# Performance work log

Measured on AMD Instinct MI355X. Metric: run time of the kernel, lower is better.

The kernel has to match this reference:

```python
import jax, jax.numpy as jnp
import numpy as np

B, L, D_MODEL = 2, 4096, 256
EXPAND = 2
D_INNER = EXPAND * D_MODEL
D_STATE = 16
D_CONV = 4
DT_RANK = max(1, D_MODEL // 16)


def setup_inputs() -> dict:
    key = jax.random.key(0)
    ks = jax.random.split(key, 8)
    s = 0.02
    return {
        "x": jax.random.normal(ks[0], (B, L, D_MODEL), jnp.float32),
        "in_proj_w": jax.random.normal(ks[1], (D_MODEL, 2 * D_INNER), jnp.float32) * s,
        "conv_w": jax.random.normal(ks[2], (D_INNER, D_CONV), jnp.float32) * 0.1,
        "conv_b": jnp.zeros((D_INNER,), jnp.float32),
        "x_proj_w": jax.random.normal(ks[3], (D_INNER, DT_RANK + 2 * D_STATE), jnp.float32) * s,
        "dt_proj_w": jax.random.normal(ks[4], (DT_RANK, D_INNER), jnp.float32) * (DT_RANK ** -0.5),
        "dt_proj_b": jnp.log(jnp.expm1(jnp.full((D_INNER,), 0.01, jnp.float32))),
        "A_log": jnp.log(jnp.tile(jnp.arange(1, D_STATE + 1, dtype=jnp.float32), (D_INNER, 1))),
        "D": jnp.ones((D_INNER,), jnp.float32),
        "out_proj_w": jax.random.normal(ks[5], (D_INNER, D_MODEL), jnp.float32) * s,
        "ln_gamma": jnp.ones((D_MODEL,), jnp.float32),
        "ln_beta": jnp.zeros((D_MODEL,), jnp.float32),
    }


def _mamba(x, in_proj_w, conv_w, conv_b, x_proj_w, dt_proj_w, dt_proj_b, A_log, D, out_proj_w):
    b = x.shape[0]
    xz = x @ in_proj_w                       # [B,L,2*d_inner]
    u, z = jnp.split(xz, 2, axis=-1)
    # depthwise causal conv over time
    u_pad = jnp.pad(u, ((0, 0), (D_CONV - 1, 0), (0, 0)))
    kern = conv_w.T[:, None, :]              # [D_CONV, 1, D_INNER]
    u_conv = jax.lax.conv_general_dilated(
        u_pad, kern, (1,), 'VALID',
        dimension_numbers=('NHC', 'HIO', 'NHC'),
        feature_group_count=D_INNER) + conv_b
    u_conv = jax.nn.silu(u_conv)             # [B,L,d_inner]
    dbl = u_conv @ x_proj_w
    dt, Bm, Cm = jnp.split(dbl, [DT_RANK, DT_RANK + D_STATE], axis=-1)
    delta = jax.nn.softplus(dt @ dt_proj_w + dt_proj_b)   # [B,L,d_inner]
    A = -jnp.exp(A_log)                                    # [d_inner,d_state]
    dA = jnp.exp(delta[..., None] * A)                     # [B,L,di,ds]
    dBu = delta[..., None] * Bm[:, :, None, :] * u_conv[..., None]

    def step(h, inputs):
        dA_t, dBu_t, C_t = inputs
        h = dA_t * h + dBu_t                 # [B,di,ds]
        y = jnp.einsum('bdn,bn->bd', h, C_t)
        return h, y

    h0 = jnp.zeros((b, D_INNER, D_STATE), u_conv.dtype)
    _, ys = jax.lax.scan(step, h0,
                         (dA.transpose(1, 0, 2, 3),
                          dBu.transpose(1, 0, 2, 3),
                          Cm.transpose(1, 0, 2)))
    y = ys.transpose(1, 0, 2) + u_conv * D
    y = y * jax.nn.silu(z)
    return y @ out_proj_w


def reference(x, in_proj_w, conv_w, conv_b, x_proj_w, dt_proj_w, dt_proj_b,
              A_log, D, out_proj_w, ln_gamma, ln_beta):
    y = x + _mamba(x, in_proj_w, conv_w, conv_b, x_proj_w, dt_proj_w,
                   dt_proj_b, A_log, D, out_proj_w)
    mu = jnp.mean(y, axis=-1, keepdims=True)
    var = jnp.var(y, axis=-1, keepdims=True)
    return (y - mu) / jnp.sqrt(var + 1e-5) * ln_gamma + ln_beta
```

## Files before the change

### kernel.cpp

```cpp
#include <hip/hip_runtime.h>
#include <math.h>

constexpr int BATCH  = 2;
constexpr int LSEQ   = 4096;
constexpr int DMODEL = 256;
constexpr int DINNER = 512;
constexpr int NST    = 16;
constexpr int MROWS  = BATCH * LSEQ;
constexpr int NCH    = 256;
constexpr int TCH    = LSEQ / NCH;
constexpr float LOG2E = 1.44269504088896f;
constexpr float LN2   = 0.69314718056f;

typedef __attribute__((ext_vector_type(8))) short bf16x8;
typedef __attribute__((ext_vector_type(4))) float f32x4;

__device__ __forceinline__ float fast_silu(float v) { return v / (1.f + __expf(-v)); }

__device__ __forceinline__ unsigned short f2bf(float f) {
  unsigned int u = __float_as_uint(f);
  u = (u + 0x7fffu + ((u >> 16) & 1u)) >> 16;
  return (unsigned short)u;
}
__device__ __forceinline__ float bf2f(unsigned short u) {
  return __uint_as_float(((unsigned int)u) << 16);
}

__global__ __launch_bounds__(256) void k_prep(const float* __restrict__ ipw,
                                              const float* __restrict__ opw,
                                              const float* __restrict__ xpw,
                                              const float* __restrict__ Alog,
                                              unsigned short* __restrict__ W1t,
                                              unsigned short* __restrict__ W2t,
                                              unsigned short* __restrict__ xpT,
                                              float* __restrict__ a2T) {
  __shared__ float tile[32][33];
  const int bid = blockIdx.x;
  const int t = threadIdx.x;
  if (bid < 384) {
    const float* W; unsigned short* Wt; int K, N, ktiles, bt;
    if (bid < 256) { W = ipw; Wt = W1t; K = 256; N = 1024; ktiles = 8;  bt = bid; }
    else           { W = opw; Wt = W2t; K = 512; N = 256;  ktiles = 16; bt = bid - 256; }
    const int kt = bt % ktiles, nt = bt / ktiles;
    const int k0 = kt * 32, n0 = nt * 32;
    const int c = t & 31, r0 = t >> 5;
    #pragma unroll
    for (int it = 0; it < 4; ++it) {
      int r = r0 + it * 8;
      tile[r][c] = W[(size_t)(k0 + r) * N + n0 + c];
    }
    __syncthreads();
    #pragma unroll
    for (int it = 0; it < 4; ++it) {
      int cc = r0 + it * 8;
      Wt[(size_t)(n0 + cc) * K + k0 + c] = f2bf(tile[c][cc]);
    }
  } else if (bid < 480) {
    int idx = (bid - 384) * 256 + t;
    int n = idx >> 9, k = idx & 511;
    xpT[n * 512 + k] = f2bf(xpw[k * 48 + n]);
  } else {
    int idx = (bid - 480) * 256 + t;
    int n = idx >> 9, d = idx & 511;
    a2T[idx] = -__expf(Alog[d * NST + n]) * LOG2E;
  }
}

__global__ __launch_bounds__(256) void k_inproj(const float* __restrict__ X,
                                                const unsigned short* __restrict__ Wt,
                                                unsigned short* __restrict__ ub,
                                                unsigned short* __restrict__ zb) {
  __shared__ unsigned short As[128][40];
  __shared__ unsigned short Bs[128][40];
  const int t = threadIdx.x;
  const int m0 = (blockIdx.x & 63) * 128;
  const int n0 = (blockIdx.x >> 6) * 128;
  const int lane = t & 63, wid = t >> 6;
  const int hi = lane >> 4, l15 = lane & 15;
  const int wm = wid >> 1, wn = wid & 1;
  f32x4 zero = {0.f, 0.f, 0.f, 0.f};
  f32x4 acc[4][4];
  #pragma unroll
  for (int i = 0; i < 4; ++i)
    #pragma unroll
    for (int j = 0; j < 4; ++j) acc[i][j] = zero;

  for (int k0 = 0; k0 < DMODEL; k0 += 32) {
    __syncthreads();
    #pragma unroll
    for (int it = 0; it < 4; ++it) {
      int v = it * 256 + t;
      int r = v >> 3, part = v & 7;
      float4 a = *(const float4*)(X + (size_t)(m0 + r) * 256 + k0 + part * 4);
      ushort4 o;
      o.x = f2bf(a.x); o.y = f2bf(a.y); o.z = f2bf(a.z); o.w = f2bf(a.w);
      *(ushort4*)(&As[r][part * 4]) = o;
    }
    #pragma unroll
    for (int it = 0; it < 2; ++it) {
      int v = it * 256 + t;
      int r = v >> 2, part = v & 3;
      *(float4*)(&Bs[r][part * 8]) = *(const float4*)(Wt + (size_t)(n0 + r) * 256 + k0 + part * 8);
    }
    __syncthreads();
    bf16x8 af[4], bfv[4];
    #pragma unroll
    for (int am = 0; am < 4; ++am) af[am] = *(const bf16x8*)(&As[wm * 64 + am * 16 + l15][hi * 8]);
    #pragma unroll
    for (int bn = 0; bn < 4; ++bn) bfv[bn] = *(const bf16x8*)(&Bs[wn * 64 + bn * 16 + l15][hi * 8]);
    #pragma unroll
    for (int am = 0; am < 4; ++am)
      #pragma unroll
      for (int bn = 0; bn < 4; ++bn)
        acc[am][bn] = __builtin_amdgcn_mfma_f32_16x16x32_bf16(af[am], bfv[bn], acc[am][bn], 0, 0, 0);
  }

  unsigned short* dst = (n0 < DINNER) ? ub : zb;
  const int nb = (n0 < DINNER) ? n0 : n0 - DINNER;
  #pragma unroll
  for (int am = 0; am < 4; ++am)
    #pragma unroll
    for (int j = 0; j < 4; ++j) {
      int m = m0 + wm * 64 + am * 16 + hi * 4 + j;
      #pragma unroll
      for (int bn = 0; bn < 4; ++bn) {
        int n = nb + wn * 64 + bn * 16 + l15;
        dst[(size_t)m * DINNER + n] = f2bf(acc[am][bn][j]);
      }
    }
}

__global__ __launch_bounds__(128) void k_xprojm(const unsigned short* __restrict__ ub,
                                                const float* __restrict__ cw,
                                                const float* __restrict__ cb,
                                                unsigned short* __restrict__ ucb,
                                                const unsigned short* __restrict__ xpT,
                                                float* __restrict__ dt_out,
                                                float* __restrict__ Bout,
                                                float* __restrict__ Cout) {
  __shared__ unsigned short U[35][520];
  __shared__ unsigned short Bs[48][136];
  const int t = threadIdx.x;
  const int m0 = blockIdx.x * 32;
  const int l0 = m0 & (LSEQ - 1);
  const int lane = t & 63, wid = t >> 6;
  const int hi = lane >> 4, l15 = lane & 15;

  for (int v = t; v < 35 * 64; v += 128) {
    int r = v >> 6, c8 = v & 63;
    float4 val = {0.f, 0.f, 0.f, 0.f};
    if (l0 - 3 + r >= 0)
      val = *(const float4*)(ub + (size_t)(m0 - 3 + r) * 512 + c8 * 8);
    *(float4*)(&U[r][c8 * 8]) = val;
  }
  __syncthreads();

  #pragma unroll
  for (int cc = 0; cc < 4; ++cc) {
    const int k = t * 4 + cc;
    const float w0 = cw[k * 4 + 0], w1 = cw[k * 4 + 1], w2 = cw[k * 4 + 2], w3 = cw[k * 4 + 3];
    const float bias = cb[k];
    for (int r = 31; r >= 0; --r) {
      float acc = bias;
      acc = fmaf(bf2f(U[r + 0][k]), w0, acc);
      acc = fmaf(bf2f(U[r + 1][k]), w1, acc);
      acc = fmaf(bf2f(U[r + 2][k]), w2, acc);
      acc = fmaf(bf2f(U[r + 3][k]), w3, acc);
      U[r + 3][k] = f2bf(fast_silu(acc));
    }
  }
  __syncthreads();

  for (int v = t; v < 32 * 64; v += 128) {
    int r = v >> 6, c8 = v & 63;
    *(float4*)(ucb + (size_t)(m0 + r) * 512 + c8 * 8) = *(const float4*)(&U[r + 3][c8 * 8]);
  }

  f32x4 zero = {0.f, 0.f, 0.f, 0.f};
  f32x4 acc[3] = {zero, zero, zero};
  for (int k0 = 0; k0 < DINNER; k0 += 128) {
    __syncthreads();
    #pragma unroll
    for (int it = 0; it < 6; ++it) {
      int v = it * 128 + t;
      int r = v >> 4, part = v & 15;
      *(float4*)(&Bs[r][part * 8]) = *(const float4*)(xpT + (size_t)r * 512 + k0 + part * 8);
    }
    __syncthreads();
    #pragma unroll
    for (int kk = 0; kk < 4; ++kk) {
      bf16x8 af = *(const bf16x8*)(&U[3 + wid * 16 + l15][k0 + kk * 32 + hi * 8]);
      #pragma unroll
      for (int nf = 0; nf < 3; ++nf) {
        bf16x8 bv = *(const bf16x8*)(&Bs[nf * 16 + l15][kk * 32 + hi * 8]);
        acc[nf] = __builtin_amdgcn_mfma_f32_16x16x32_bf16(af, bv, acc[nf], 0, 0, 0);
      }
    }
  }
  #pragma unroll
  for (int j = 0; j < 4; ++j) {
    int m = m0 + wid * 16 + hi * 4 + j;
    dt_out[m * 16 + l15] = acc[0][j];
    Bout[m * 16 + l15]   = acc[1][j];
    Cout[m * 16 + l15]   = acc[2][j];
  }
}

__global__ __launch_bounds__(256) void k_scan1(const unsigned short* __restrict__ ucb,
                                               const float* __restrict__ dtin,
                                               const float* __restrict__ dtw,
                                               const float* __restrict__ dtb,
                                               const float* __restrict__ Bin,
                                               const float* __restrict__ a2T,
                                               unsigned short* __restrict__ delta_b,
                                               unsigned short* __restrict__ Ssum,
                                               float* __restrict__ Dsum) {
  const int t = threadIdx.x;
  const int d0 = (blockIdx.x & 1) * 256;
  const int rest = blockIdx.x >> 1;
  const int c = rest & (NCH - 1);
  const int b = rest >> 8;
  const int d = d0 + t;
  __shared__ float Bsh[TCH][NST];
  __shared__ float dtsh[TCH][NST];
  __shared__ unsigned short UC[TCH][256];
  const int rbase = (b * LSEQ + c * TCH) * DINNER + d0;
  {
    const int base = (b * LSEQ + c * TCH) * NST;
    ((float*)Bsh)[t]  = Bin[base + t];
    ((float*)dtsh)[t] = dtin[base + t];
    #pragma unroll
    for (int it = 0; it < 2; ++it) {
      int v = it * 256 + t;
      int r = v >> 5, col8 = v & 31;
      *(float4*)(&UC[r][col8 * 8]) = *(const float4*)(ucb + rbase + r * DINNER + col8 * 8);
    }
  }
  __syncthreads();
  float dwreg[NST];
  #pragma unroll
  for (int r = 0; r < NST; ++r) dwreg[r] = dtw[r * DINNER + d];
  const float bias = dtb[d];
  float a2[NST];
  #pragma unroll
  for (int n = 0; n < NST; ++n) a2[n] = a2T[n * DINNER + d];
  bool geo = true;
  #pragma unroll
  for (int n = 1; n < NST; ++n)
    geo = geo && (fabsf(a2[n] - (float)(n + 1) * a2[0]) <= 1e-5f * fabsf(a2[n]));
  float S[NST];
  #pragma unroll
  for (int n = 0; n < NST; ++n) S[n] = 0.f;
  float dsum = 0.f;
  const int row0 = rbase + t;
  for (int tt = 0; tt < TCH; ++tt) {
    float acc = bias;
    #pragma unroll
    for (int r = 0; r < NST; ++r) acc = fmaf(dtsh[tt][r], dwreg[r], acc);
    float sp = (acc > 20.f) ? acc : __logf(1.f + __expf(acc));
    unsigned short deb = f2bf(sp);
    delta_b[row0 + tt * DINNER] = deb;
    float de = bf2f(deb);
    float xv = bf2f(UC[tt][t]);
    float du = de * xv;
    dsum += de;
    float dA[NST];
    if (geo) {
      float r1 = exp2f(de * a2[0]);
      float p = r1;
      #pragma unroll
      for (int n = 0; n < NST; ++n) { dA[n] = p; p *= r1; }
    } else {
      #pragma unroll
      for (int n = 0; n < NST; ++n) dA[n] = exp2f(de * a2[n]);
    }
    #pragma unroll
    for (int n = 0; n < NST; ++n) S[n] = fmaf(dA[n], S[n], du * Bsh[tt][n]);
  }
  const int bc = b * NCH + c;
  Dsum[bc * DINNER + d] = dsum;
  #pragma unroll
  for (int n = 0; n < NST; ++n)
    Ssum[(size_t)((n * BATCH + b) * NCH + c) * DINNER + d] = f2bf(S[n]);
}

__global__ __launch_bounds__(64) void k_scan2(const unsigned short* __restrict__ S,
                                              const float* __restrict__ Dsum,
                                              const float* __restrict__ a2T,
                                              unsigned short* __restrict__ Hinit) {
  const int idx = blockIdx.x * 64 + threadIdx.x;
  const int d  = idx & (DINNER - 1);
  const int nb = idx >> 9;
  const int b  = nb & (BATCH - 1);
  const int n  = nb >> 1;
  const float a = a2T[n * DINNER + d] * LN2;
  const unsigned short* Srow = S     + (size_t)nb * NCH * DINNER + d;
  const float*          Drow = Dsum  + (size_t)b  * NCH * DINNER + d;
  unsigned short*       Hrow = Hinit + (size_t)nb * NCH * DINNER + d;
  float h = 0.f;
  #pragma unroll 8
  for (int c = 0; c < NCH; ++c) {
    float ds = Drow[(size_t)c * DINNER];
    float s  = bf2f(Srow[(size_t)c * DINNER]);
    Hrow[(size_t)c * DINNER] = f2bf(h);
    h = fmaf(__expf(a * ds), h, s);
  }
}

__global__ __launch_bounds__(256) void k_scan3(const unsigned short* __restrict__ ucb,
                                               const unsigned short* __restrict__ delta_b,
                                               const float* __restrict__ Bin,
                                               const float* __restrict__ Cin,
                                               const float* __restrict__ a2T,
                                               const float* __restrict__ Dvec,
                                               const unsigned short* __restrict__ Hinit,
                                               unsigned short* __restrict__ zb) {
  const int t = threadIdx.x;
  const int d0 = (blockIdx.x & 1) * 256;
  const int rest = blockIdx.x >> 1;
  const int c = rest & (NCH - 1);
  const int b = rest >> 8;
  const int d = d0 + t;
  __shared__ float Bsh[TCH][NST];
  __shared__ float Csh[TCH][NST];
  __shared__ unsigned short UC[TCH][256];
  __shared__ unsigned short DE[TCH][256];
  const int rbase = (b * LSEQ + c * TCH) * DINNER + d0;
  {
    const int base = (b * LSEQ + c * TCH) * NST;
    ((float*)Bsh)[t] = Bin[base + t];
    ((float*)Csh)[t] = Cin[base + t];
    #pragma unroll
    for (int it = 0; it < 2; ++it) {
      int v = it * 256 + t;
      int r = v >> 5, col8 = v & 31;
      *(float4*)(&UC[r][col8 * 8]) = *(const float4*)(ucb     + rbase + r * DINNER + col8 * 8);
      *(float4*)(&DE[r][col8 * 8]) = *(const float4*)(delta_b + rbase + r * DINNER + col8 * 8);
    }
  }
  __syncthreads();
  float a2[NST];
  #pragma unroll
  for (int n = 0; n < NST; ++n) a2[n] = a2T[n * DINNER + d];
  bool geo = true;
  #pragma unroll
  for (int n = 1; n < NST; ++n)
    geo = geo && (fabsf(a2[n] - (float)(n + 1) * a2[0]) <= 1e-5f * fabsf(a2[n]));
  float h[NST];
  #pragma unroll
  for (int n = 0; n < NST; ++n)
    h[n] = bf2f(Hinit[(size_t)(((n * BATCH + b) * NCH) + c) * DINNER + d]);
  const float Dd = Dvec[d];
  const int row0 = rbase + t;
  for (int tt = 0; tt < TCH; ++tt) {
    float de = bf2f(DE[tt][t]);
    float xv = bf2f(UC[tt][t]);
    float du = de * xv;
    float dA[NST];
    if (geo) {
      float r1 = exp2f(de * a2[0]);
      float p = r1;
      #pragma unroll
      for (int n = 0; n < NST; ++n) { dA[n] = p; p *= r1; }
    } else {
      #pragma unroll
      for (int n = 0; n < NST; ++n) dA[n] = exp2f(de * a2[n]);
    }
    float y = 0.f;
    #pragma unroll
    for (int n = 0; n < NST; ++n) {
      h[n] = fmaf(dA[n], h[n], du * Bsh[tt][n]);
      y = fmaf(h[n], Csh[tt][n], y);
    }
    float zz = bf2f(zb[row0 + tt * DINNER]);
    zb[row0 + tt * DINNER] = f2bf((y + xv * Dd) * fast_silu(zz));
  }
}

__global__ __launch_bounds__(512) void k_out(const unsigned short* __restrict__ Yb,
                                             const unsigned short* __restrict__ W2t,
                                             const float* __restrict__ X,
                                             const float* __restrict__ gam,
                                             const float* __restrict__ bet,
                                             float* __restrict__ out) {
  __shared__ unsigned short As[32][40];
  __shared__ unsigned short Bs[256][40];
  __shared__ float red[4][32][2];
  const int t = threadIdx.x;
  const int m0 = blockIdx.x * 32;
  const int lane = t & 63, wid = t >> 6;
  const int hi = lane >> 4, l15 = lane & 15;
  const int wm = wid >> 2, wn = wid & 3;
  f32x4 zero = {0.f, 0.f, 0.f, 0.f};
  f32x4 acc[4];
  #pragma unroll
  for (int bn = 0; bn < 4; ++bn) acc[bn] = zero;

  for (int k0 = 0; k0 < DINNER; k0 += 32) {
    __syncthreads();
    if (t < 128) {
      int r = t >> 2, part = t & 3;
      *(float4*)(&As[r][part * 8]) = *(const float4*)(Yb + (size_t)(m0 + r) * 512 + k0 + part * 8);
    }
    #pragma unroll
    for (int it = 0; it < 2; ++it) {
      int v = it * 512 + t;
      int r = v >> 2, part = v & 3;
      *(float4*)(&Bs[r][part * 8]) = *(const float4*)(W2t + (size_t)r * 512 + k0 + part * 8);
    }
    __syncthreads();
    bf16x8 af = *(const bf16x8*)(&As[wm * 16 + l15][hi * 8]);
    #pragma unroll
    for (int bn = 0; bn < 4; ++bn) {
      bf16x8 bfr = *(const bf16x8*)(&Bs[wn * 64 + bn * 16 + l15][hi * 8]);
      acc[bn] = __builtin_amdgcn_mfma_f32_16x16x32_bf16(af, bfr, acc[bn], 0, 0, 0);
    }
  }

  float vv[4][4];
  float s[4] = {0.f, 0.f, 0.f, 0.f}, s2[4] = {0.f, 0.f, 0.f, 0.f};
  #pragma unroll
  for (int bn = 0; bn < 4; ++bn) {
    int n = wn * 64 + bn * 16 + l15;
    #pragma unroll
    for (int j = 0; j < 4; ++j) {
      int m = m0 + wm * 16 + hi * 4 + j;
      float v = acc[bn][j] + X[(size_t)m * DMODEL + n];
      vv[bn][j] = v;
      s[j] += v; s2[j] += v * v;
    }
  }
  #pragma unroll
  for (int j = 0; j < 4; ++j) {
    #pragma unroll
    for (int off = 1; off < 16; off <<= 1) {
      s[j]  += __shfl_xor(s[j],  off, 64);
      s2[j] += __shfl_xor(s2[j], off, 64);
    }
  }
  if (l15 == 0) {
    #pragma unroll
    for (int j = 0; j < 4; ++j) {
      red[wn][wm * 16 + hi * 4 + j][0] = s[j];
      red[wn][wm * 16 + hi * 4 + j][1] = s2[j];
    }
  }
  __syncthreads();
  float g[4], bb[4];
  #pragma unroll
  for (int bn = 0; bn < 4; ++bn) {
    int n = wn * 64 + bn * 16 + l15;
    g[bn] = gam[n]; bb[bn] = bet[n];
  }
  #pragma unroll
  for (int j = 0; j < 4; ++j) {
    int row = wm * 16 + hi * 4 + j;
    float S  = red[0][row][0] + red[1][row][0] + red[2][row][0] + red[3][row][0];
    float S2 = red[0][row][1] + red[1][row][1] + red[2][row][1] + red[3][row][1];
    float mu = S * (1.f / 256.f);
    float rstd = rsqrtf(S2 * (1.f / 256.f) - mu * mu + 1e-5f);
    int m = m0 + row;
    #pragma unroll
    for (int bn = 0; bn < 4; ++bn) {
      int n = wn * 64 + bn * 16 + l15;
      out[(size_t)m * DMODEL + n] = (vv[bn][j] - mu) * rstd * g[bn] + bb[bn];
    }
  }
}

extern "C" void kernel_launch(void* const* d_in, const int* in_sizes, int n_in,
                              void* d_out, int out_size, void* d_ws, size_t ws_size,
                              hipStream_t stream) {
  const float* x    = (const float*)d_in[0];
  const float* ipw  = (const float*)d_in[1];
  const float* cw   = (const float*)d_in[2];
  const float* cb   = (const float*)d_in[3];
  const float* xpw  = (const float*)d_in[4];
  const float* dtw  = (const float*)d_in[5];
  const float* dtbv = (const float*)d_in[6];
  const float* alog = (const float*)d_in[7];
  const float* Dv   = (const float*)d_in[8];
  const float* opw  = (const float*)d_in[9];
  const float* gam  = (const float*)d_in[10];
  const float* bet  = (const float*)d_in[11];
  float* out = (float*)d_out;

  char* ws = (char*)d_ws;
  unsigned short* ub  = (unsigned short*)ws;   ws += (size_t)MROWS * DINNER * 2;
  unsigned short* zb  = (unsigned short*)ws;   ws += (size_t)MROWS * DINNER * 2;
  unsigned short* ucb = (unsigned short*)ws;   ws += (size_t)MROWS * DINNER * 2;
  float* buf_dt = (float*)ws;  ws += (size_t)MROWS * NST * 4;
  float* buf_B  = (float*)ws;  ws += (size_t)MROWS * NST * 4;
  float* buf_C  = (float*)ws;  ws += (size_t)MROWS * NST * 4;
  float* buf_ds = (float*)ws;  ws += (size_t)BATCH * NCH * DINNER * 4;
  unsigned short* buf_S = (unsigned short*)ws;  ws += (size_t)NST * BATCH * NCH * DINNER * 2;
  unsigned short* buf_H = (unsigned short*)ws;  ws += (size_t)NST * BATCH * NCH * DINNER * 2;
  unsigned short* W1t = (unsigned short*)ws; ws += (size_t)1024 * 256 * 2;
  unsigned short* W2t = (unsigned short*)ws; ws += (size_t)256 * 512 * 2;
  unsigned short* xpT = (unsigned short*)ws; ws += (size_t)48 * 512 * 2;
  float* a2T = (float*)ws;     ws += (size_t)NST * DINNER * 4;
  unsigned short* deltab = ub;

  k_prep   <<<dim3(512),  dim3(256), 0, stream>>>(ipw, opw, xpw, alog, W1t, W2t, xpT, a2T);
  k_inproj <<<dim3(512),  dim3(256), 0, stream>>>(x, W1t, ub, zb);
  k_xprojm <<<dim3(MROWS / 32), dim3(128), 0, stream>>>(ub, cw, cb, ucb, xpT, buf_dt, buf_B, buf_C);
  k_scan1  <<<dim3(BATCH * NCH * 2), dim3(256), 0, stream>>>(ucb, buf_dt, dtw, dtbv, buf_B,
                                                             a2T, deltab, buf_S, buf_ds);
  k_scan2  <<<dim3(NST * BATCH * DINNER / 64), dim3(64), 0, stream>>>(buf_S, buf_ds, a2T, buf_H);
  k_scan3  <<<dim3(BATCH * NCH * 2), dim3(256), 0, stream>>>(ucb, deltab, buf_B, buf_C,
                                                             a2T, Dv, buf_H, zb);
  k_out    <<<dim3(MROWS / 32), dim3(512), 0, stream>>>(zb, W2t, x, gam, bet, out);
}
```

Before: 111.0 us.

## Fuse three-phase chunked scan into one cooperative kernel with grid syncs

Replaces the scan1/scan2/scan3 kernel sequence with a single cooperative kernel of 512 blocks by 512 threads. Each block keeps its chunk's u_conv, delta, B, C and dt in shared memory across phases, separated by grid-wide syncs. This avoids two kernel launches and the global round-trip of delta and u_conv between phases. The cost is two grid barriers and a middle phase where only 32 blocks run a serial 256-step prefix while the rest of the grid sits idle. The old three-kernel path remains as a fallback if occupancy is insufficient or the cooperative launch fails.

Result: no change. 111.2 us (+0.2%).

```diff
diff --git a/kernel.cpp b/kernel.cpp
--- a/kernel.cpp
+++ b/kernel.cpp
@@ -1,5 +1,8 @@
 #include <hip/hip_runtime.h>
+#include <hip/hip_cooperative_groups.h>
 #include <math.h>
+
+namespace cg = cooperative_groups;
 
 constexpr int BATCH  = 2;
 constexpr int LSEQ   = 4096;
@@ -203,6 +206,148 @@
     dt_out[m * 16 + l15] = acc[0][j];
     Bout[m * 16 + l15]   = acc[1][j];
     Cout[m * 16 + l15]   = acc[2][j];
+  }
+}
+
+__global__ __launch_bounds__(512) void k_scanf2(const unsigned short* __restrict__ ucb,
+                                                const float* __restrict__ dtin,
+                                                const float* __restrict__ dtw,
+                                                const float* __restrict__ dtb,
+                                                const float* __restrict__ Bin,
+                                                const float* __restrict__ Cin,
+                                                const float* __restrict__ a2T,
+                                                const float* __restrict__ Dvec,
+                                                unsigned short* __restrict__ Ssum,
+                                                float* __restrict__ Dsum,
+                                                unsigned short* __restrict__ Hinit,
+                                                unsigned short* __restrict__ zb) {
+  const int t = threadIdx.x;
+  const int c = blockIdx.x & (NCH - 1);
+  const int b = blockIdx.x >> 8;
+  const int d = t;
+  __shared__ float Bsh[TCH][NST];
+  __shared__ float Csh[TCH][NST];
+  __shared__ float dtsh[TCH][NST];
+  __shared__ unsigned short UC[TCH][512];
+  __shared__ unsigned short DE[TCH][512];
+  const int rbase = (b * LSEQ + c * TCH) * DINNER;
+  {
+    const int base = (b * LSEQ + c * TCH) * NST;
+    if (t < 256) {
+      ((float*)Bsh)[t]  = Bin[base + t];
+      ((float*)Csh)[t]  = Cin[base + t];
+      ((float*)dtsh)[t] = dtin[base + t];
+    }
+    #pragma unroll
+    for (int it = 0; it < 2; ++it) {
+      int v = it * 512 + t;
+      int r = v >> 6, col8 = v & 63;
+      *(float4*)(&UC[r][col8 * 8]) = *(const float4*)(ucb + rbase + r * DINNER + col8 * 8);
+    }
+  }
+  __syncthreads();
+
+  float a2[NST];
+  #pragma unroll
+  for (int n = 0; n < NST; ++n) a2[n] = a2T[n * DINNER + d];
+  bool geo = true;
+  #pragma unroll
+  for (int n = 1; n < NST; ++n)
+    geo = geo && (fabsf(a2[n] - (float)(n + 1) * a2[0]) <= 1e-5f * fabsf(a2[n]));
+
+  {
+    float dwreg[NST];
+    #pragma unroll
+    for (int r = 0; r < NST; ++r) dwreg[r] = dtw[r * DINNER + d];
+    const float bias = dtb[d];
+    float S[NST];
+    #pragma unroll
+    for (int n = 0; n < NST; ++n) S[n] = 0.f;
+    float dsum = 0.f;
+    for (int tt = 0; tt < TCH; ++tt) {
+      float acc = bias;
+      #pragma unroll
+      for (int r = 0; r < NST; ++r) acc = fmaf(dtsh[tt][r], dwreg[r], acc);
+      float sp = (acc > 20.f) ? acc : __logf(1.f + __expf(acc));
+      unsigned short deb = f2bf(sp);
+      DE[tt][t] = deb;
+      float de = bf2f(deb);
+      float xv = bf2f(UC[tt][t]);
+      float du = de * xv;
+      dsum += de;
+      float dA[NST];
+      if (geo) {
+        float r1 = exp2f(de * a2[0]);
+        float p = r1;
+        #pragma unroll
+        for (int n = 0; n < NST; ++n) { dA[n] = p; p *= r1; }
+      } else {
+        #pragma unroll
+        for (int n = 0; n < NST; ++n) dA[n] = exp2f(de * a2[n]);
+      }
+      #pragma unroll
+      for (int n = 0; n < NST; ++n) S[n] = fmaf(dA[n], S[n], du * Bsh[tt][n]);
+    }
+    Dsum[(b * NCH + c) * DINNER + d] = dsum;
+    #pragma unroll
+    for (int n = 0; n < NST; ++n)
+      Ssum[(size_t)((n * BATCH + b) * NCH + c) * DINNER + d] = f2bf(S[n]);
+  }
+  __threadfence();
+  cg::this_grid().sync();
+
+  if (blockIdx.x < 32) {
+    const int idx = blockIdx.x * 512 + t;
+    const int dd  = idx & (DINNER - 1);
+    const int nb  = idx >> 9;
+    const int bb  = nb & (BATCH - 1);
+    const int nn  = nb >> 1;
+    const float a = a2T[nn * DINNER + dd] * LN2;
+    const unsigned short* Srow = Ssum  + (size_t)nb * NCH * DINNER + dd;
+    const float*          Drow = Dsum  + (size_t)bb * NCH * DINNER + dd;
+    unsigned short*       Hrow = Hinit + (size_t)nb * NCH * DINNER + dd;
+    float h = 0.f;
+    #pragma unroll 8
+    for (int cc = 0; cc < NCH; ++cc) {
+      float ds = Drow[(size_t)cc * DINNER];
+      float s  = bf2f(Srow[(size_t)cc * DINNER]);
+      Hrow[(size_t)cc * DINNER] = f2bf(h);
+      h = fmaf(__expf(a * ds), h, s);
+    }
+  }
+  __threadfence();
+  cg::this_grid().sync();
+
+  {
+    float h[NST];
+    #pragma unroll
+    for (int n = 0; n < NST; ++n)
+      h[n] = bf2f(Hinit[(size_t)(((n * BATCH + b) * NCH) + c) * DINNER + d]);
+    const float Dd = Dvec[d];
+    const int row0 = rbase + d;
+    for (int tt = 0; tt < TCH; ++tt) {
+      float de = bf2f(DE[tt][t]);
+      float xv = bf2f(UC[tt][t]);
+      float du = de * xv;
+      float dA[NST];
+      if (geo) {
+        float r1 = exp2f(de * a2[0]);
+        float p = r1;
+        #pragma unroll
+        for (int n = 0; n < NST; ++n) { dA[n] = p; p *= r1; }
+      } else {
+        #pragma unroll
+        for (int n = 0; n < NST; ++n) dA[n] = exp2f(de * a2[n]);
+      }
+      float y = 0.f;
+      #pragma unroll
+      for (int n = 0; n < NST; ++n) {
+        h[n] = fmaf(dA[n], h[n], du * Bsh[tt][n]);
+        y = fmaf(h[n], Csh[tt][n], y);
+      }
+      float zz = bf2f(zb[row0 + tt * DINNER]);
+      zb[row0 + tt * DINNER] = f2bf((y + xv * Dd) * fast_silu(zz));
+    }
   }
 }
 
@@ -277,8 +422,7 @@
     #pragma unroll
     for (int n = 0; n < NST; ++n) S[n] = fmaf(dA[n], S[n], du * Bsh[tt][n]);
   }
-  const int bc = b * NCH + c;
-  Dsum[bc * DINNER + d] = dsum;
+  Dsum[(b * NCH + c) * DINNER + d] = dsum;
   #pragma unroll
   for (int n = 0; n < NST; ++n)
     Ssum[(size_t)((n * BATCH + b) * NCH + c) * DINNER + d] = f2bf(S[n]);
@@ -504,10 +648,31 @@
   k_prep   <<<dim3(512),  dim3(256), 0, stream>>>(ipw, opw, xpw, alog, W1t, W2t, xpT, a2T);
   k_inproj <<<dim3(512),  dim3(256), 0, stream>>>(x, W1t, ub, zb);
   k_xprojm <<<dim3(MROWS / 32), dim3(128), 0, stream>>>(ub, cw, cb, ucb, xpT, buf_dt, buf_B, buf_C);
-  k_scan1  <<<dim3(BATCH * NCH * 2), dim3(256), 0, stream>>>(ucb, buf_dt, dtw, dtbv, buf_B,
-                                                             a2T, deltab, buf_S, buf_ds);
-  k_scan2  <<<dim3(NST * BATCH * DINNER / 64), dim3(64), 0, stream>>>(buf_S, buf_ds, a2T, buf_H);
-  k_scan3  <<<dim3(BATCH * NCH * 2), dim3(256), 0, stream>>>(ucb, deltab, buf_B, buf_C,
-                                                             a2T, Dv, buf_H, zb);
+
+  bool coop = false;
+  int maxB = 0;
+  if (hipOccupancyMaxActiveBlocksPerMultiprocessor(&maxB, k_scanf2, 512, 0) == hipSuccess && maxB >= 2) {
+    const unsigned short* a_ucb = ucb;
+    const float* a_dt = buf_dt; const float* a_dtw = dtw; const float* a_dtb = dtbv;
+    const float* a_B = buf_B;   const float* a_C = buf_C; const float* a_a2 = a2T;
+    const float* a_Dv = Dv;
+    unsigned short* a_S = buf_S; float* a_ds = buf_ds; unsigned short* a_H = buf_H;
+    unsigned short* a_zb = zb;
+    void* args[] = {(void*)&a_ucb, (void*)&a_dt, (void*)&a_dtw, (void*)&a_dtb,
+                    (void*)&a_B, (void*)&a_C, (void*)&a_a2, (void*)&a_Dv,
+                    (void*)&a_S, (void*)&a_ds, (void*)&a_H, (void*)&a_zb};
+    hipError_t e = hipLaunchCooperativeKernel((void*)k_scanf2, dim3(BATCH * NCH), dim3(512),
+                                              args, 0, stream);
+    if (e == hipSuccess) coop = true;
+    else (void)hipGetLastError();
+  }
+  if (!coop) {
+    k_scan1 <<<dim3(BATCH * NCH * 2), dim3(256), 0, stream>>>(ucb, buf_dt, dtw, dtbv, buf_B,
+                                                              a2T, deltab, buf_S, buf_ds);
+    k_scan2 <<<dim3(NST * BATCH * DINNER / 64), dim3(64), 0, stream>>>(buf_S, buf_ds, a2T, buf_H);
+    k_scan3 <<<dim3(BATCH * NCH * 2), dim3(256), 0, stream>>>(ucb, deltab, buf_B, buf_C,
+                                                              a2T, Dv, buf_H, zb);
+  }
+
   k_out    <<<dim3(MROWS / 32), dim3(512), 0, stream>>>(zb, W2t, x, gam, bet, out);
 }
```
